# Optimization experiments

Measured on AMD Instinct MI355X. Metric: run time of the kernel, lower is better.

Reference implementation:

```python
import jax, jax.numpy as jnp
import numpy as np

N = 16384   # nodes
E = 262144  # edges (avg degree 16)
H = 256     # hidden_dim
R = 32      # num_radial


def _lin(k, fi, fo):
    return jax.random.normal(k, (fi, fo), jnp.float32) / np.float32(np.sqrt(fi))


def setup_inputs() -> dict:
    key = jax.random.key(0)
    ks = jax.random.split(key, 16)
    h = jax.random.normal(ks[0], (N, H), jnp.float32)
    pos = jax.random.normal(ks[1], (N, 3), jnp.float32)
    edge_index = jax.random.randint(ks[2], (2, E), 0, N, dtype=jnp.int32)
    return {
        'h': h, 'pos': pos,
        # radial_basis: Linear(1,R), SiLU, Linear(R,R)
        'rb_w1': _lin(ks[3], 1, R), 'rb_b1': jnp.zeros((R,), jnp.float32),
        'rb_w2': _lin(ks[4], R, R), 'rb_b2': jnp.zeros((R,), jnp.float32),
        # edge_network: Linear(2H+R,H), SiLU, Linear(H,H), LayerNorm(H)
        'en_w1': _lin(ks[5], 2 * H + R, H), 'en_b1': jnp.zeros((H,), jnp.float32),
        'en_w2': _lin(ks[6], H, H), 'en_b2': jnp.zeros((H,), jnp.float32),
        'en_g': jnp.ones((H,), jnp.float32), 'en_bt': jnp.zeros((H,), jnp.float32),
        # node_network: Linear(2H,H), SiLU, Linear(H,H), LayerNorm(H)
        'nn_w1': _lin(ks[7], 2 * H, H), 'nn_b1': jnp.zeros((H,), jnp.float32),
        'nn_w2': _lin(ks[8], H, H), 'nn_b2': jnp.zeros((H,), jnp.float32),
        'nn_g': jnp.ones((H,), jnp.float32), 'nn_bt': jnp.zeros((H,), jnp.float32),
        # coord_network: Linear(H,H//2), SiLU, Linear(H//2,1), Tanh
        'cn_w1': _lin(ks[9], H, H // 2), 'cn_b1': jnp.zeros((H // 2,), jnp.float32),
        'cn_w2': _lin(ks[10], H // 2, 1), 'cn_b2': jnp.zeros((1,), jnp.float32),
        'edge_index': edge_index,
    }


def _ln(x, g, b, eps=1e-5):
    mu = jnp.mean(x, axis=-1, keepdims=True)
    var = jnp.var(x, axis=-1, keepdims=True)
    return (x - mu) / jnp.sqrt(var + eps) * g + b


def reference(h, pos, rb_w1, rb_b1, rb_w2, rb_b2,
              en_w1, en_b1, en_w2, en_b2, en_g, en_bt,
              nn_w1, nn_b1, nn_w2, nn_b2, nn_g, nn_bt,
              cn_w1, cn_b1, cn_w2, cn_b2, edge_index):
    row, col = edge_index[0], edge_index[1]
    rel_pos = pos[col] - pos[row]                                   # [E,3]
    # torch: norm(rel_pos + 1e-8) -> scalar eps added to the vector first
    dist = jnp.linalg.norm(rel_pos + 1e-8, axis=-1, keepdims=True)  # [E,1]
    radial = jax.nn.silu(dist @ rb_w1 + rb_b1) @ rb_w2 + rb_b2      # [E,R]
    edge_feat = jnp.concatenate([h[row], h[col], radial], axis=-1)  # [E,2H+R]
    edge_msg = _ln(jax.nn.silu(edge_feat @ en_w1 + en_b1) @ en_w2 + en_b2,
                   en_g, en_bt)                                     # [E,H]
    # PyG propagate with aggr='add': sum messages at target nodes (col)
    node_msg = jax.ops.segment_sum(edge_msg, col, num_segments=h.shape[0])
    hn_in = jnp.concatenate([h, node_msg], axis=-1)                 # [N,2H]
    h_updated = _ln(jax.nn.silu(hn_in @ nn_w1 + nn_b1) @ nn_w2 + nn_b2,
                    nn_g, nn_bt)                                    # [N,H]
    coord_w = jnp.tanh(jax.nn.silu(edge_msg @ cn_w1 + cn_b1) @ cn_w2 + cn_b2)  # [E,1]
    weighted = rel_pos * coord_w                                    # [E,3]
    pos_updates = jnp.zeros_like(pos).at[row].add(-weighted).at[col].add(weighted)
    return h_updated, pos_updates
```

## Files before the change

kernel.cpp:

```cpp
#include <hip/hip_runtime.h>
#include <hip/hip_bf16.h>


#define NN 16384
#define EE 262144
#define HH 256
#define RR 32

typedef __bf16 bf16x8 __attribute__((ext_vector_type(8)));
typedef float f32x4 __attribute__((ext_vector_type(4)));

__device__ __forceinline__ float silu_f(float x) { return x / (1.0f + __expf(-x)); }

__global__ __launch_bounds__(256) void conv_h_kernel(const float* __restrict__ src,
                                                     __hip_bfloat16* __restrict__ dst,
                                                     int n4) {
  int i = blockIdx.x * 256 + threadIdx.x;
  if (i >= n4) return;
  float4 v = ((const float4*)src)[i];
  __hip_bfloat16* d = dst + (size_t)i * 4;
  d[0] = __float2bfloat16(v.x);
  d[1] = __float2bfloat16(v.y);
  d[2] = __float2bfloat16(v.z);
  d[3] = __float2bfloat16(v.w);
}

__global__ __launch_bounds__(256) void tr_kernel(const float* __restrict__ in,
                                                 __hip_bfloat16* __restrict__ out,
                                                 int K, int Nc) {
  int i = blockIdx.x * 256 + threadIdx.x;
  if (i >= K * Nc) return;
  int k = i / Nc, c = i - k * Nc;
  out[(size_t)c * K + k] = __float2bfloat16(in[i]);
}

__global__ __launch_bounds__(256) void rwt_kernel(const float* __restrict__ rb_w2,
                                                  const float* __restrict__ en_w1,
                                                  __hip_bfloat16* __restrict__ RWT) {
  int t = blockIdx.x * 256 + threadIdx.x;
  if (t >= 256 * 32) return;
  int c = t >> 5, i = t & 31;
  float s = 0.f;
#pragma unroll
  for (int j = 0; j < 32; ++j) s += rb_w2[i * 32 + j] * en_w1[(512 + j) * 256 + c];
  RWT[c * 32 + i] = __float2bfloat16(s);
}

__global__ __launch_bounds__(256) void b1p_kernel(const float* __restrict__ en_b1,
                                                  const float* __restrict__ rb_b2,
                                                  const float* __restrict__ en_w1,
                                                  float* __restrict__ b1p) {
  int c = blockIdx.x * 256 + threadIdx.x;
  if (c >= 256) return;
  float s = en_b1[c];
#pragma unroll
  for (int j = 0; j < 32; ++j) s += rb_b2[j] * en_w1[(512 + j) * 256 + c];
  b1p[c] = s;
}

__global__ __launch_bounds__(256) void count_kernel(const int* __restrict__ ei,
                                                    int* __restrict__ counts) {
  int e = blockIdx.x * 256 + threadIdx.x;
  if (e >= EE) return;
  atomicAdd(&counts[ei[EE + e]], 1);
}

__global__ __launch_bounds__(1024) void scan_kernel(const int* __restrict__ counts,
                                                    int* __restrict__ offs,
                                                    int* __restrict__ cursor) {
  __shared__ int buf[1024];
  __shared__ int carry;
  int tid = threadIdx.x;
  if (tid == 0) carry = 0;
  __syncthreads();
  for (int base = 0; base < NN; base += 1024) {
    int v = counts[base + tid];
    buf[tid] = v;
    __syncthreads();
    for (int s = 1; s < 1024; s <<= 1) {
      int x = (tid >= s) ? buf[tid - s] : 0;
      __syncthreads();
      buf[tid] += x;
      __syncthreads();
    }
    int incl = buf[tid];
    int c = carry;
    __syncthreads();
    offs[base + tid] = c + incl - v;
    cursor[base + tid] = c + incl - v;
    if (tid == 1023) carry = c + incl;
    __syncthreads();
  }
  if (tid == 0) offs[NN] = carry;
}

__global__ __launch_bounds__(256) void scatter_kernel(const int* __restrict__ ei,
                                                      int* __restrict__ cursor,
                                                      int* __restrict__ elist) {
  int e = blockIdx.x * 256 + threadIdx.x;
  if (e >= EE) return;
  int c = ei[EE + e];
  int p = atomicAdd(&cursor[c], 1);
  elist[p] = e;
}

__global__ __launch_bounds__(512) void pgemm_kernel(const __hip_bfloat16* __restrict__ A,
                                                    const __hip_bfloat16* __restrict__ BT,
                                                    __hip_bfloat16* __restrict__ out) {
  const int tid = threadIdx.x, w = tid >> 6, l = tid & 63, r = l & 15, g = l >> 4;
  const int n0 = blockIdx.x * 64;
  f32x4 acc[4][4];
#pragma unroll
  for (int a = 0; a < 4; ++a)
#pragma unroll
    for (int b = 0; b < 4; ++b) acc[a][b] = (f32x4){0.f, 0.f, 0.f, 0.f};
  for (int ks = 0; ks < 8; ++ks) {
    bf16x8 af[4], bfr[4];
#pragma unroll
    for (int fm = 0; fm < 4; ++fm)
      af[fm] = *(const bf16x8*)(A + (size_t)(n0 + fm * 16 + r) * 256 + ks * 32 + g * 8);
#pragma unroll
    for (int fn = 0; fn < 4; ++fn)
      bfr[fn] = *(const bf16x8*)(BT + (size_t)(w * 64 + fn * 16 + r) * 256 + ks * 32 + g * 8);
#pragma unroll
    for (int fm = 0; fm < 4; ++fm)
#pragma unroll
      for (int fn = 0; fn < 4; ++fn)
        acc[fm][fn] =
            __builtin_amdgcn_mfma_f32_16x16x32_bf16(af[fm], bfr[fn], acc[fm][fn], 0, 0, 0);
  }
#pragma unroll
  for (int fm = 0; fm < 4; ++fm)
#pragma unroll
    for (int fn = 0; fn < 4; ++fn) {
      int col = w * 64 + fn * 16 + r;
#pragma unroll
      for (int q = 0; q < 4; ++q) {
        int row = n0 + fm * 16 + g * 4 + q;
        out[(size_t)row * 512 + col] = __float2bfloat16(acc[fm][fn][q]);
      }
    }
}

__global__ __launch_bounds__(512, 4) void edge_kernel(
    const __hip_bfloat16* __restrict__ Pb, const int* __restrict__ ei,
    const float* __restrict__ pos, const float* __restrict__ rb_w1,
    const float* __restrict__ rb_b1, const __hip_bfloat16* __restrict__ RWT,
    const float* __restrict__ b1p, const __hip_bfloat16* __restrict__ W2T,
    const float* __restrict__ en_b2, const float* __restrict__ en_g,
    const float* __restrict__ en_bt, const __hip_bfloat16* __restrict__ CW1T,
    const float* __restrict__ cn_b1, const float* __restrict__ cn_w2,
    const float* __restrict__ cn_b2, __hip_bfloat16* __restrict__ emsg,
    float* __restrict__ pos_out) {
  __shared__ __align__(16) __hip_bfloat16 A2[64 * 264];
  __shared__ float distb[64];
  __shared__ float relb[64][3];
  __shared__ int srow[64], scol[64];
  __shared__ float wc1[32], bc1[32];
  __shared__ float red[8][64], redsq[8][64], red2[8][64];
  __shared__ float mv[64][2];
  __shared__ float gb[HH], btb[HH], cb1b[128], cw2b[128];

  const int tid = threadIdx.x, w = tid >> 6, l = tid & 63, r = l & 15, g = l >> 4;
  const int e0 = blockIdx.x * 64;

  if (tid < 256) {
    gb[tid] = en_g[tid];
    btb[tid] = en_bt[tid];
  }
  if (tid < 128) {
    cb1b[tid] = cn_b1[tid];
    cw2b[tid] = cn_w2[tid];
  }
  if (tid < 32) {
    wc1[tid] = rb_w1[tid];
    bc1[tid] = rb_b1[tid];
  }
  if (tid < 64) {
    int e = e0 + tid;
    int rr = ei[e], cc = ei[EE + e];
    srow[tid] = rr;
    scol[tid] = cc;
    float dx = pos[cc * 3 + 0] - pos[rr * 3 + 0];
    float dy = pos[cc * 3 + 1] - pos[rr * 3 + 1];
    float dz = pos[cc * 3 + 2] - pos[rr * 3 + 2];
    relb[tid][0] = dx;
    relb[tid][1] = dy;
    relb[tid][2] = dz;
    float ex = dx + 1e-8f, ey = dy + 1e-8f, ez = dz + 1e-8f;
    distb[tid] = sqrtf(ex * ex + ey * ey + ez * ez);
  }
  __syncthreads();

#pragma unroll
  for (int it = 0; it < 4; ++it) {
    int ch = it * 512 + tid;
    int i = ch >> 5, c = ch & 31;
    bf16x8 p1 = *(const bf16x8*)(Pb + (size_t)srow[i] * 512 + c * 8);
    bf16x8 p2 = *(const bf16x8*)(Pb + (size_t)scol[i] * 512 + 256 + c * 8);
    bf16x8 o;
#pragma unroll
    for (int j = 0; j < 8; ++j) o[j] = (__bf16)((float)p1[j] + (float)p2[j]);
    *(bf16x8*)(A2 + i * 264 + c * 8) = o;
  }

  f32x4 acc[4][2];
  {
    bf16x8 sf[4], bfr[2];
#pragma unroll
    for (int fm = 0; fm < 4; ++fm) {
      float d = distb[fm * 16 + r];
      bf16x8 v;
#pragma unroll
      for (int j = 0; j < 8; ++j) {
        float x = d * wc1[g * 8 + j] + bc1[g * 8 + j];
        v[j] = (__bf16)silu_f(x);
      }
      sf[fm] = v;
    }
#pragma unroll
    for (int fn = 0; fn < 2; ++fn)
      bfr[fn] = *(const bf16x8*)(RWT + (size_t)(w * 32 + fn * 16 + r) * 32 + g * 8);
#pragma unroll
    for (int fm = 0; fm < 4; ++fm)
#pragma unroll
      for (int fn = 0; fn < 2; ++fn)
        acc[fm][fn] = __builtin_amdgcn_mfma_f32_16x16x32_bf16(
            sf[fm], bfr[fn], (f32x4){0.f, 0.f, 0.f, 0.f}, 0, 0, 0);
  }
  __syncthreads();

#pragma unroll
  for (int fn = 0; fn < 2; ++fn) {
    int col = w * 32 + fn * 16 + r;
    float bp = b1p[col];
#pragma unroll
    for (int fm = 0; fm < 4; ++fm)
#pragma unroll
      for (int q = 0; q < 4; ++q) {
        int row = fm * 16 + g * 4 + q;
        float ps = __bfloat162float(A2[row * 264 + col]);
        A2[row * 264 + col] = __float2bfloat16(silu_f(acc[fm][fn][q] + ps + bp));
      }
  }
  __syncthreads();

#pragma unroll
  for (int a = 0; a < 4; ++a)
#pragma unroll
    for (int b = 0; b < 2; ++b) acc[a][b] = (f32x4){0.f, 0.f, 0.f, 0.f};
  for (int ks = 0; ks < 8; ++ks) {
    bf16x8 af[4], bfr[2];
#pragma unroll
    for (int fm = 0; fm < 4; ++fm)
      af[fm] = *(const bf16x8*)(A2 + (fm * 16 + r) * 264 + ks * 32 + g * 8);
#pragma unroll
    for (int fn = 0; fn < 2; ++fn)
      bfr[fn] = *(const bf16x8*)(W2T + (size_t)(w * 32 + fn * 16 + r) * 256 + ks * 32 + g * 8);
#pragma unroll
    for (int fm = 0; fm < 4; ++fm)
#pragma unroll
      for (int fn = 0; fn < 2; ++fn)
        acc[fm][fn] =
            __builtin_amdgcn_mfma_f32_16x16x32_bf16(af[fm], bfr[fn], acc[fm][fn], 0, 0, 0);
  }
#pragma unroll
  for (int fn = 0; fn < 2; ++fn) {
    float b2 = en_b2[w * 32 + fn * 16 + r];
#pragma unroll
    for (int fm = 0; fm < 4; ++fm)
#pragma unroll
      for (int q = 0; q < 4; ++q) acc[fm][fn][q] += b2;
  }

#pragma unroll
  for (int fm = 0; fm < 4; ++fm)
#pragma unroll
    for (int q = 0; q < 4; ++q) {
      float s = acc[fm][0][q] + acc[fm][1][q];
      float sq = acc[fm][0][q] * acc[fm][0][q] + acc[fm][1][q] * acc[fm][1][q];
#pragma unroll
      for (int m = 1; m < 16; m <<= 1) {
        s += __shfl_xor(s, m, 64);
        sq += __shfl_xor(sq, m, 64);
      }
      if (r == 0) {
        red[w][fm * 16 + g * 4 + q] = s;
        redsq[w][fm * 16 + g * 4 + q] = sq;
      }
    }
  __syncthreads();
  if (tid < 64) {
    float s = 0.f, sq = 0.f;
#pragma unroll
    for (int k = 0; k < 8; ++k) {
      s += red[k][tid];
      sq += redsq[k][tid];
    }
    float mean = s * (1.0f / HH);
    float var = sq * (1.0f / HH) - mean * mean;
    mv[tid][0] = mean;
    mv[tid][1] = rsqrtf(var + 1e-5f);
  }
  __syncthreads();
#pragma unroll
  for (int fn = 0; fn < 2; ++fn) {
    int col = w * 32 + fn * 16 + r;
    float gg = gb[col], bb = btb[col];
#pragma unroll
    for (int fm = 0; fm < 4; ++fm)
#pragma unroll
      for (int q = 0; q < 4; ++q) {
        int row = fm * 16 + g * 4 + q;
        A2[row * 264 + col] =
            __float2bfloat16((acc[fm][fn][q] - mv[row][0]) * mv[row][1] * gg + bb);
      }
  }
  __syncthreads();

#pragma unroll
  for (int it = 0; it < 4; ++it) {
    int ch = it * 512 + tid;
    int i = ch >> 5, c = ch & 31;
    *(float4*)(emsg + (size_t)(e0 + i) * HH + c * 8) = *(const float4*)(A2 + i * 264 + c * 8);
  }

  f32x4 c2[4];
#pragma unroll
  for (int a = 0; a < 4; ++a) c2[a] = (f32x4){0.f, 0.f, 0.f, 0.f};
  for (int ks = 0; ks < 8; ++ks) {
    bf16x8 af[4];
#pragma unroll
    for (int fm = 0; fm < 4; ++fm)
      af[fm] = *(const bf16x8*)(A2 + (fm * 16 + r) * 264 + ks * 32 + g * 8);
    bf16x8 bfr = *(const bf16x8*)(CW1T + (size_t)(w * 16 + r) * 256 + ks * 32 + g * 8);
#pragma unroll
    for (int fm = 0; fm < 4; ++fm)
      c2[fm] = __builtin_amdgcn_mfma_f32_16x16x32_bf16(af[fm], bfr, c2[fm], 0, 0, 0);
  }
  {
    int ccol = w * 16 + r;
    float cb = cb1b[ccol], cw = cw2b[ccol];
#pragma unroll
    for (int fm = 0; fm < 4; ++fm)
#pragma unroll
      for (int q = 0; q < 4; ++q) {
        float v = silu_f(c2[fm][q] + cb) * cw;
#pragma unroll
        for (int m = 1; m < 16; m <<= 1) v += __shfl_xor(v, m, 64);
        if (r == 0) red2[w][fm * 16 + g * 4 + q] = v;
      }
  }
  __syncthreads();
  if (tid < 64) {
    float s = cn_b2[0];
#pragma unroll
    for (int k = 0; k < 8; ++k) s += red2[k][tid];
    float wgt = tanhf(s);
    float ax = relb[tid][0], ay = relb[tid][1], az = relb[tid][2];
    int rr = srow[tid], cc = scol[tid];
    atomicAdd(&pos_out[rr * 3 + 0], -wgt * ax);
    atomicAdd(&pos_out[rr * 3 + 1], -wgt * ay);
    atomicAdd(&pos_out[rr * 3 + 2], -wgt * az);
    atomicAdd(&pos_out[cc * 3 + 0], wgt * ax);
    atomicAdd(&pos_out[cc * 3 + 1], wgt * ay);
    atomicAdd(&pos_out[cc * 3 + 2], wgt * az);
  }
}

__global__ __launch_bounds__(256) void nodemsg_kernel(const int* __restrict__ offs,
                                                      const int* __restrict__ elist,
                                                      const __hip_bfloat16* __restrict__ emsg,
                                                      __hip_bfloat16* __restrict__ nmsgb) {
  int wid = threadIdx.x >> 6, l = threadIdx.x & 63;
  int n = blockIdx.x * 4 + wid;
  float a0 = 0.f, a1 = 0.f, a2 = 0.f, a3 = 0.f;
  int b = offs[n], e2 = offs[n + 1];
  for (int idx = b; idx < e2; ++idx) {
    int e = elist[idx];
    const __hip_bfloat16* row = emsg + (size_t)e * HH;
    a0 += __bfloat162float(row[l]);
    a1 += __bfloat162float(row[l + 64]);
    a2 += __bfloat162float(row[l + 128]);
    a3 += __bfloat162float(row[l + 192]);
  }
  __hip_bfloat16* out = nmsgb + (size_t)n * HH;
  out[l] = __float2bfloat16(a0);
  out[l + 64] = __float2bfloat16(a1);
  out[l + 128] = __float2bfloat16(a2);
  out[l + 192] = __float2bfloat16(a3);
}

__global__ __launch_bounds__(512, 4) void node_kernel(
    const __hip_bfloat16* __restrict__ hb, const __hip_bfloat16* __restrict__ nmsgb,
    const __hip_bfloat16* __restrict__ NW1T, const float* __restrict__ nn_b1,
    const __hip_bfloat16* __restrict__ NW2T, const float* __restrict__ nn_b2,
    const float* __restrict__ nn_g, const float* __restrict__ nn_bt,
    float* __restrict__ out_h) {
  __shared__ __align__(16) __hip_bfloat16 A2[32 * 264];
  __shared__ float red[8][32], redsq[8][32];
  __shared__ float mv[32][2];
  __shared__ float gb[HH], btb[HH];
  const int tid = threadIdx.x, w = tid >> 6, l = tid & 63, r = l & 15, g = l >> 4;
  const int n0 = blockIdx.x * 32;
  if (tid < 256) {
    gb[tid] = nn_g[tid];
    btb[tid] = nn_bt[tid];
  }

  f32x4 acc[2][2];
#pragma unroll
  for (int a = 0; a < 2; ++a)
#pragma unroll
    for (int b = 0; b < 2; ++b) acc[a][b] = (f32x4){0.f, 0.f, 0.f, 0.f};
  for (int ks = 0; ks < 8; ++ks) {
    bf16x8 af[2], bfr[2];
#pragma unroll
    for (int fm = 0; fm < 2; ++fm)
      af[fm] = *(const bf16x8*)(hb + (size_t)(n0 + fm * 16 + r) * 256 + ks * 32 + g * 8);
#pragma unroll
    for (int fn = 0; fn < 2; ++fn)
      bfr[fn] = *(const bf16x8*)(NW1T + (size_t)(w * 32 + fn * 16 + r) * 512 + ks * 32 + g * 8);
#pragma unroll
    for (int fm = 0; fm < 2; ++fm)
#pragma unroll
      for (int fn = 0; fn < 2; ++fn)
        acc[fm][fn] =
            __builtin_amdgcn_mfma_f32_16x16x32_bf16(af[fm], bfr[fn], acc[fm][fn], 0, 0, 0);
  }
  for (int ks = 0; ks < 8; ++ks) {
    bf16x8 af[2], bfr[2];
#pragma unroll
    for (int fm = 0; fm < 2; ++fm)
      af[fm] = *(const bf16x8*)(nmsgb + (size_t)(n0 + fm * 16 + r) * 256 + ks * 32 + g * 8);
#pragma unroll
    for (int fn = 0; fn < 2; ++fn)
      bfr[fn] = *(const bf16x8*)(NW1T + (size_t)(w * 32 + fn * 16 + r) * 512 + 256 + ks * 32 + g * 8);
#pragma unroll
    for (int fm = 0; fm < 2; ++fm)
#pragma unroll
      for (int fn = 0; fn < 2; ++fn)
        acc[fm][fn] =
            __builtin_amdgcn_mfma_f32_16x16x32_bf16(af[fm], bfr[fn], acc[fm][fn], 0, 0, 0);
  }
  __syncthreads();
#pragma unroll
  for (int fn = 0; fn < 2; ++fn) {
    int col = w * 32 + fn * 16 + r;
    float b1 = nn_b1[col];
#pragma unroll
    for (int fm = 0; fm < 2; ++fm)
#pragma unroll
      for (int q = 0; q < 4; ++q) {
        int row = fm * 16 + g * 4 + q;
        A2[row * 264 + col] = __float2bfloat16(silu_f(acc[fm][fn][q] + b1));
      }
  }
  __syncthreads();

#pragma unroll
  for (int a = 0; a < 2; ++a)
#pragma unroll
    for (int b = 0; b < 2; ++b) acc[a][b] = (f32x4){0.f, 0.f, 0.f, 0.f};
  for (int ks = 0; ks < 8; ++ks) {
    bf16x8 af[2], bfr[2];
#pragma unroll
    for (int fm = 0; fm < 2; ++fm)
      af[fm] = *(const bf16x8*)(A2 + (fm * 16 + r) * 264 + ks * 32 + g * 8);
#pragma unroll
    for (int fn = 0; fn < 2; ++fn)
      bfr[fn] = *(const bf16x8*)(NW2T + (size_t)(w * 32 + fn * 16 + r) * 256 + ks * 32 + g * 8);
#pragma unroll
    for (int fm = 0; fm < 2; ++fm)
#pragma unroll
      for (int fn = 0; fn < 2; ++fn)
        acc[fm][fn] =
            __builtin_amdgcn_mfma_f32_16x16x32_bf16(af[fm], bfr[fn], acc[fm][fn], 0, 0, 0);
  }
#pragma unroll
  for (int fn = 0; fn < 2; ++fn) {
    float b2 = nn_b2[w * 32 + fn * 16 + r];
#pragma unroll
    for (int fm = 0; fm < 2; ++fm)
#pragma unroll
      for (int q = 0; q < 4; ++q) acc[fm][fn][q] += b2;
  }
#pragma unroll
  for (int fm = 0; fm < 2; ++fm)
#pragma unroll
    for (int q = 0; q < 4; ++q) {
      float s = acc[fm][0][q] + acc[fm][1][q];
      float sq = acc[fm][0][q] * acc[fm][0][q] + acc[fm][1][q] * acc[fm][1][q];
#pragma unroll
      for (int m = 1; m < 16; m <<= 1) {
        s += __shfl_xor(s, m, 64);
        sq += __shfl_xor(sq, m, 64);
      }
      if (r == 0) {
        red[w][fm * 16 + g * 4 + q] = s;
        redsq[w][fm * 16 + g * 4 + q] = sq;
      }
    }
  __syncthreads();
  if (tid < 32) {
    float s = 0.f, sq = 0.f;
#pragma unroll
    for (int k = 0; k < 8; ++k) {
      s += red[k][tid];
      sq += redsq[k][tid];
    }
    float mean = s * (1.0f / HH);
    float var = sq * (1.0f / HH) - mean * mean;
    mv[tid][0] = mean;
    mv[tid][1] = rsqrtf(var + 1e-5f);
  }
  __syncthreads();
#pragma unroll
  for (int fn = 0; fn < 2; ++fn) {
    int col = w * 32 + fn * 16 + r;
    float gg = gb[col], bb = btb[col];
#pragma unroll
    for (int fm = 0; fm < 2; ++fm)
#pragma unroll
      for (int q = 0; q < 4; ++q) {
        int row = fm * 16 + g * 4 + q;
        out_h[(size_t)(n0 + row) * HH + col] =
            (acc[fm][fn][q] - mv[row][0]) * mv[row][1] * gg + bb;
      }
  }
}

extern "C" void kernel_launch(void* const* d_in, const int* in_sizes, int n_in,
                              void* d_out, int out_size, void* d_ws, size_t ws_size,
                              hipStream_t stream) {
  const float* h = (const float*)d_in[0];
  const float* pos = (const float*)d_in[1];
  const float* rb_w1 = (const float*)d_in[2];
  const float* rb_b1 = (const float*)d_in[3];
  const float* rb_w2 = (const float*)d_in[4];
  const float* rb_b2 = (const float*)d_in[5];
  const float* en_w1 = (const float*)d_in[6];
  const float* en_b1 = (const float*)d_in[7];
  const float* en_w2 = (const float*)d_in[8];
  const float* en_b2 = (const float*)d_in[9];
  const float* en_g = (const float*)d_in[10];
  const float* en_bt = (const float*)d_in[11];
  const float* nn_w1 = (const float*)d_in[12];
  const float* nn_b1 = (const float*)d_in[13];
  const float* nn_w2 = (const float*)d_in[14];
  const float* nn_b2 = (const float*)d_in[15];
  const float* nn_g = (const float*)d_in[16];
  const float* nn_bt = (const float*)d_in[17];
  const float* cn_w1 = (const float*)d_in[18];
  const float* cn_b1 = (const float*)d_in[19];
  const float* cn_w2 = (const float*)d_in[20];
  const float* cn_b2 = (const float*)d_in[21];
  const int* ei = (const int*)d_in[22];

  float* out_h = (float*)d_out;
  float* out_pos = out_h + (size_t)NN * HH;

  char* p = (char*)d_ws;
  auto alloc = [&p](size_t bytes) {
    char* q = p;
    p += (bytes + 255) & ~(size_t)255;
    return q;
  };
  __hip_bfloat16* hb = (__hip_bfloat16*)alloc((size_t)NN * HH * 2);
  __hip_bfloat16* Pb = (__hip_bfloat16*)alloc((size_t)NN * 512 * 2);
  __hip_bfloat16* W1abT = (__hip_bfloat16*)alloc((size_t)512 * 256 * 2);
  __hip_bfloat16* W2T = (__hip_bfloat16*)alloc((size_t)256 * 256 * 2);
  __hip_bfloat16* NW1T = (__hip_bfloat16*)alloc((size_t)256 * 512 * 2);
  __hip_bfloat16* NW2T = (__hip_bfloat16*)alloc((size_t)256 * 256 * 2);
  __hip_bfloat16* CW1T = (__hip_bfloat16*)alloc((size_t)128 * 256 * 2);
  __hip_bfloat16* RWT = (__hip_bfloat16*)alloc((size_t)256 * 32 * 2);
  float* b1p = (float*)alloc((size_t)256 * 4);
  __hip_bfloat16* emsg = (__hip_bfloat16*)alloc((size_t)EE * HH * 2);
  __hip_bfloat16* nmsgb = (__hip_bfloat16*)alloc((size_t)NN * HH * 2);
  int* counts = (int*)alloc((size_t)NN * 4);
  int* offs = (int*)alloc((size_t)(NN + 1) * 4);
  int* cursor = (int*)alloc((size_t)NN * 4);
  int* elist = (int*)alloc((size_t)EE * 4);

  hipMemsetAsync(out_pos, 0, (size_t)NN * 3 * sizeof(float), stream);
  hipMemsetAsync(counts, 0, (size_t)NN * sizeof(int), stream);

  conv_h_kernel<<<(NN * HH / 4 + 255) / 256, 256, 0, stream>>>(h, hb, NN * HH / 4);
  tr_kernel<<<(256 * 256) / 256, 256, 0, stream>>>(en_w2, W2T, 256, 256);
  tr_kernel<<<(512 * 256) / 256, 256, 0, stream>>>(nn_w1, NW1T, 512, 256);
  tr_kernel<<<(256 * 256) / 256, 256, 0, stream>>>(nn_w2, NW2T, 256, 256);
  tr_kernel<<<(256 * 128) / 256, 256, 0, stream>>>(cn_w1, CW1T, 256, 128);
  tr_kernel<<<(256 * 256) / 256, 256, 0, stream>>>(en_w1, W1abT, 256, 256);
  tr_kernel<<<(256 * 256) / 256, 256, 0, stream>>>(en_w1 + 256 * 256, W1abT + 256 * 256, 256,
                                                   256);
  rwt_kernel<<<(256 * 32) / 256, 256, 0, stream>>>(rb_w2, en_w1, RWT);
  b1p_kernel<<<1, 256, 0, stream>>>(en_b1, rb_b2, en_w1, b1p);
  count_kernel<<<EE / 256, 256, 0, stream>>>(ei, counts);
  scan_kernel<<<1, 1024, 0, stream>>>(counts, offs, cursor);
  scatter_kernel<<<EE / 256, 256, 0, stream>>>(ei, cursor, elist);
  pgemm_kernel<<<NN / 64, 512, 0, stream>>>(hb, W1abT, Pb);
  edge_kernel<<<EE / 64, 512, 0, stream>>>(Pb, ei, pos, rb_w1, rb_b1, RWT, b1p, W2T, en_b2,
                                           en_g, en_bt, CW1T, cn_b1, cn_w2, cn_b2, emsg,
                                           out_pos);
  nodemsg_kernel<<<NN / 4, 256, 0, stream>>>(offs, elist, emsg, nmsgb);
  node_kernel<<<NN / 32, 512, 0, stream>>>(hb, nmsgb, NW1T, nn_b1, NW2T, nn_b2, nn_g, nn_bt,
                                           out_h);
}
```

Baseline: 526.1 us.

## Fuse radial MFMA into edge gather, parallelize scan, vectorize node message sum

```diff
diff --git a/kernel.cpp b/kernel.cpp
--- a/kernel.cpp
+++ b/kernel.cpp
@@ -11,6 +11,15 @@
 typedef float f32x4 __attribute__((ext_vector_type(4)));
 
 __device__ __forceinline__ float silu_f(float x) { return x / (1.0f + __expf(-x)); }
+
+__device__ __forceinline__ unsigned short bf_bits(float x) {
+  union { __hip_bfloat16 b; unsigned short u; } v;
+  v.b = __float2bfloat16(x);
+  return v.u;
+}
+__device__ __forceinline__ float ubf(unsigned short u) {
+  return __uint_as_float(((unsigned)u) << 16);
+}
 
 __global__ __launch_bounds__(256) void conv_h_kernel(const float* __restrict__ src,
                                                      __hip_bfloat16* __restrict__ dst,
@@ -65,33 +74,52 @@
   atomicAdd(&counts[ei[EE + e]], 1);
 }
 
-__global__ __launch_bounds__(1024) void scan_kernel(const int* __restrict__ counts,
+__global__ __launch_bounds__(256) void scanA_kernel(const int* __restrict__ counts,
+                                                    int* __restrict__ bsum) {
+  __shared__ int ws[4];
+  int t = threadIdx.x;
+  int v = counts[blockIdx.x * 256 + t];
+#pragma unroll
+  for (int m = 1; m < 64; m <<= 1) v += __shfl_xor(v, m, 64);
+  if ((t & 63) == 0) ws[t >> 6] = v;
+  __syncthreads();
+  if (t == 0) bsum[blockIdx.x] = ws[0] + ws[1] + ws[2] + ws[3];
+}
+
+__global__ __launch_bounds__(64) void scanB_kernel(const int* __restrict__ bsum,
+                                                   int* __restrict__ bbase,
+                                                   int* __restrict__ offs) {
+  int t = threadIdx.x;
+  int v = bsum[t], x = v;
+#pragma unroll
+  for (int d = 1; d < 64; d <<= 1) {
+    int y = __shfl_up(x, d, 64);
+    if (t >= d) x += y;
+  }
+  bbase[t] = x - v;
+  if (t == 63) offs[NN] = x;
+}
+
+__global__ __launch_bounds__(256) void scanC_kernel(const int* __restrict__ counts,
+                                                    const int* __restrict__ bbase,
                                                     int* __restrict__ offs,
                                                     int* __restrict__ cursor) {
-  __shared__ int buf[1024];
-  __shared__ int carry;
-  int tid = threadIdx.x;
-  if (tid == 0) carry = 0;
-  __syncthreads();
-  for (int base = 0; base < NN; base += 1024) {
-    int v = counts[base + tid];
-    buf[tid] = v;
-    __syncthreads();
-    for (int s = 1; s < 1024; s <<= 1) {
-      int x = (tid >= s) ? buf[tid - s] : 0;
-      __syncthreads();
-      buf[tid] += x;
-      __syncthreads();
-    }
-    int incl = buf[tid];
-    int c = carry;
-    __syncthreads();
-    offs[base + tid] = c + incl - v;
-    cursor[base + tid] = c + incl - v;
-    if (tid == 1023) carry = c + incl;
-    __syncthreads();
-  }
-  if (tid == 0) offs[NN] = carry;
+  __shared__ int wtot[4];
+  int t = threadIdx.x, wv = t >> 6, ln = t & 63;
+  int base = blockIdx.x * 256;
+  int v = counts[base + t], x = v;
+#pragma unroll
+  for (int d = 1; d < 64; d <<= 1) {
+    int y = __shfl_up(x, d, 64);
+    if (ln >= d) x += y;
+  }
+  if (ln == 63) wtot[wv] = x;
+  __syncthreads();
+  int add = bbase[blockIdx.x];
+  for (int k = 0; k < wv; ++k) add += wtot[k];
+  int excl = add + x - v;
+  offs[base + t] = excl;
+  cursor[base + t] = excl;
 }
 
 __global__ __launch_bounds__(256) void scatter_kernel(const int* __restrict__ ei,
@@ -153,16 +181,29 @@
     const float* __restrict__ cn_b2, __hip_bfloat16* __restrict__ emsg,
     float* __restrict__ pos_out) {
   __shared__ __align__(16) __hip_bfloat16 A2[64 * 264];
-  __shared__ float distb[64];
   __shared__ float relb[64][3];
   __shared__ int srow[64], scol[64];
-  __shared__ float wc1[32], bc1[32];
-  __shared__ float red[8][64], redsq[8][64], red2[8][64];
+  __shared__ float red[8][64], redsq[8][64];
   __shared__ float mv[64][2];
   __shared__ float gb[HH], btb[HH], cb1b[128], cw2b[128];
 
   const int tid = threadIdx.x, w = tid >> 6, l = tid & 63, r = l & 15, g = l >> 4;
   const int e0 = blockIdx.x * 64;
+  const int chalf = w >> 2;
+
+  const int eloc = (w & 3) * 16 + r;
+  const int eg = e0 + eloc;
+  const int nr = ei[eg], nc = ei[EE + eg];
+  float dx = pos[nc * 3 + 0] - pos[nr * 3 + 0] + 1e-8f;
+  float dy = pos[nc * 3 + 1] - pos[nr * 3 + 1] + 1e-8f;
+  float dz = pos[nc * 3 + 2] - pos[nr * 3 + 2] + 1e-8f;
+  float d = sqrtf(dx * dx + dy * dy + dz * dz);
+  bf16x8 sfrag;
+#pragma unroll
+  for (int j = 0; j < 8; ++j) {
+    float x = d * rb_w1[g * 8 + j] + rb_b1[g * 8 + j];
+    sfrag[j] = (__bf16)silu_f(x);
+  }
 
   if (tid < 256) {
     gb[tid] = en_g[tid];
@@ -172,79 +213,38 @@
     cb1b[tid] = cn_b1[tid];
     cw2b[tid] = cn_w2[tid];
   }
-  if (tid < 32) {
-    wc1[tid] = rb_w1[tid];
-    bc1[tid] = rb_b1[tid];
-  }
   if (tid < 64) {
     int e = e0 + tid;
-    int rr = ei[e], cc = ei[EE + e];
-    srow[tid] = rr;
-    scol[tid] = cc;
-    float dx = pos[cc * 3 + 0] - pos[rr * 3 + 0];
-    float dy = pos[cc * 3 + 1] - pos[rr * 3 + 1];
-    float dz = pos[cc * 3 + 2] - pos[rr * 3 + 2];
-    relb[tid][0] = dx;
-    relb[tid][1] = dy;
-    relb[tid][2] = dz;
-    float ex = dx + 1e-8f, ey = dy + 1e-8f, ez = dz + 1e-8f;
-    distb[tid] = sqrtf(ex * ex + ey * ey + ez * ez);
-  }
-  __syncthreads();
-
-#pragma unroll
-  for (int it = 0; it < 4; ++it) {
-    int ch = it * 512 + tid;
-    int i = ch >> 5, c = ch & 31;
-    bf16x8 p1 = *(const bf16x8*)(Pb + (size_t)srow[i] * 512 + c * 8);
-    bf16x8 p2 = *(const bf16x8*)(Pb + (size_t)scol[i] * 512 + 256 + c * 8);
-    bf16x8 o;
-#pragma unroll
-    for (int j = 0; j < 8; ++j) o[j] = (__bf16)((float)p1[j] + (float)p2[j]);
-    *(bf16x8*)(A2 + i * 264 + c * 8) = o;
-  }
+    int r2 = ei[e], c2 = ei[EE + e];
+    srow[tid] = r2;
+    scol[tid] = c2;
+    relb[tid][0] = pos[c2 * 3 + 0] - pos[r2 * 3 + 0];
+    relb[tid][1] = pos[c2 * 3 + 1] - pos[r2 * 3 + 1];
+    relb[tid][2] = pos[c2 * 3 + 2] - pos[r2 * 3 + 2];
+  }
+
+  const unsigned short* Pu = (const unsigned short*)Pb;
+  unsigned short* A2u = (unsigned short*)A2;
+#pragma unroll
+  for (int t = 0; t < 8; ++t) {
+    int cblk = chalf * 8 + t;
+    int cbase = cblk * 16 + g * 4;
+    bf16x8 afr = *(const bf16x8*)(RWT + (size_t)(cblk * 16 + r) * 32 + g * 8);
+    f32x4 rad = __builtin_amdgcn_mfma_f32_16x16x32_bf16(afr, sfrag,
+                                                        (f32x4){0.f, 0.f, 0.f, 0.f}, 0, 0, 0);
+    ushort4 p1 = *(const ushort4*)(Pu + (size_t)nr * 512 + cbase);
+    ushort4 p2 = *(const ushort4*)(Pu + (size_t)nc * 512 + 256 + cbase);
+    float4 b1v = *(const float4*)(b1p + cbase);
+    ushort4 o;
+    o.x = bf_bits(silu_f(rad[0] + ubf(p1.x) + ubf(p2.x) + b1v.x));
+    o.y = bf_bits(silu_f(rad[1] + ubf(p1.y) + ubf(p2.y) + b1v.y));
+    o.z = bf_bits(silu_f(rad[2] + ubf(p1.z) + ubf(p2.z) + b1v.z));
+    o.w = bf_bits(silu_f(rad[3] + ubf(p1.w) + ubf(p2.w) + b1v.w));
+    *(ushort4*)(A2u + (size_t)eloc * 264 + cbase) = o;
+  }
+  __syncthreads();
 
   f32x4 acc[4][2];
-  {
-    bf16x8 sf[4], bfr[2];
-#pragma unroll
-    for (int fm = 0; fm < 4; ++fm) {
-      float d = distb[fm * 16 + r];
-      bf16x8 v;
-#pragma unroll
-      for (int j = 0; j < 8; ++j) {
-        float x = d * wc1[g * 8 + j] + bc1[g * 8 + j];
-        v[j] = (__bf16)silu_f(x);
-      }
-      sf[fm] = v;
-    }
-#pragma unroll
-    for (int fn = 0; fn < 2; ++fn)
-      bfr[fn] = *(const bf16x8*)(RWT + (size_t)(w * 32 + fn * 16 + r) * 32 + g * 8);
-#pragma unroll
-    for (int fm = 0; fm < 4; ++fm)
-#pragma unroll
-      for (int fn = 0; fn < 2; ++fn)
-        acc[fm][fn] = __builtin_amdgcn_mfma_f32_16x16x32_bf16(
-            sf[fm], bfr[fn], (f32x4){0.f, 0.f, 0.f, 0.f}, 0, 0, 0);
-  }
-  __syncthreads();
-
-#pragma unroll
-  for (int fn = 0; fn < 2; ++fn) {
-    int col = w * 32 + fn * 16 + r;
-    float bp = b1p[col];
-#pragma unroll
-    for (int fm = 0; fm < 4; ++fm)
-#pragma unroll
-      for (int q = 0; q < 4; ++q) {
-        int row = fm * 16 + g * 4 + q;
-        float ps = __bfloat162float(A2[row * 264 + col]);
-        A2[row * 264 + col] = __float2bfloat16(silu_f(acc[fm][fn][q] + ps + bp));
-      }
-  }
-  __syncthreads();
-
 #pragma unroll
   for (int a = 0; a < 4; ++a)
 #pragma unroll
@@ -325,9 +325,9 @@
     *(float4*)(emsg + (size_t)(e0 + i) * HH + c * 8) = *(const float4*)(A2 + i * 264 + c * 8);
   }
 
-  f32x4 c2[4];
-#pragma unroll
-  for (int a = 0; a < 4; ++a) c2[a] = (f32x4){0.f, 0.f, 0.f, 0.f};
+  f32x4 c2a[4];
+#pragma unroll
+  for (int a = 0; a < 4; ++a) c2a[a] = (f32x4){0.f, 0.f, 0.f, 0.f};
   for (int ks = 0; ks < 8; ++ks) {
     bf16x8 af[4];
 #pragma unroll
@@ -336,7 +336,7 @@
     bf16x8 bfr = *(const bf16x8*)(CW1T + (size_t)(w * 16 + r) * 256 + ks * 32 + g * 8);
 #pragma unroll
     for (int fm = 0; fm < 4; ++fm)
-      c2[fm] = __builtin_amdgcn_mfma_f32_16x16x32_bf16(af[fm], bfr, c2[fm], 0, 0, 0);
+      c2a[fm] = __builtin_amdgcn_mfma_f32_16x16x32_bf16(af[fm], bfr, c2a[fm], 0, 0, 0);
   }
   {
     int ccol = w * 16 + r;
@@ -345,17 +345,17 @@
     for (int fm = 0; fm < 4; ++fm)
 #pragma unroll
       for (int q = 0; q < 4; ++q) {
-        float v = silu_f(c2[fm][q] + cb) * cw;
+        float v = silu_f(c2a[fm][q] + cb) * cw;
 #pragma unroll
         for (int m = 1; m < 16; m <<= 1) v += __shfl_xor(v, m, 64);
-        if (r == 0) red2[w][fm * 16 + g * 4 + q] = v;
+        if (r == 0) red[w][fm * 16 + g * 4 + q] = v;
       }
   }
   __syncthreads();
   if (tid < 64) {
     float s = cn_b2[0];
 #pragma unroll
-    for (int k = 0; k < 8; ++k) s += red2[k][tid];
+    for (int k = 0; k < 8; ++k) s += red[k][tid];
     float wgt = tanhf(s);
     float ax = relb[tid][0], ay = relb[tid][1], az = relb[tid][2];
     int rr = srow[tid], cc = scol[tid];
@@ -376,19 +376,31 @@
   int n = blockIdx.x * 4 + wid;
   float a0 = 0.f, a1 = 0.f, a2 = 0.f, a3 = 0.f;
   int b = offs[n], e2 = offs[n + 1];
-  for (int idx = b; idx < e2; ++idx) {
-    int e = elist[idx];
-    const __hip_bfloat16* row = emsg + (size_t)e * HH;
-    a0 += __bfloat162float(row[l]);
-    a1 += __bfloat162float(row[l + 64]);
-    a2 += __bfloat162float(row[l + 128]);
-    a3 += __bfloat162float(row[l + 192]);
-  }
-  __hip_bfloat16* out = nmsgb + (size_t)n * HH;
-  out[l] = __float2bfloat16(a0);
-  out[l + 64] = __float2bfloat16(a1);
-  out[l + 128] = __float2bfloat16(a2);
-  out[l + 192] = __float2bfloat16(a3);
+  const unsigned short* E = (const unsigned short*)emsg;
+  int idx = b;
+  for (; idx + 1 < e2; idx += 2) {
+    int ea = elist[idx], eb = elist[idx + 1];
+    ushort4 va = *(const ushort4*)(E + (size_t)ea * HH + l * 4);
+    ushort4 vb = *(const ushort4*)(E + (size_t)eb * HH + l * 4);
+    a0 += ubf(va.x) + ubf(vb.x);
+    a1 += ubf(va.y) + ubf(vb.y);
+    a2 += ubf(va.z) + ubf(vb.z);
+    a3 += ubf(va.w) + ubf(vb.w);
+  }
+  if (idx < e2) {
+    int ea = elist[idx];
+    ushort4 va = *(const ushort4*)(E + (size_t)ea * HH + l * 4);
+    a0 += ubf(va.x);
+    a1 += ubf(va.y);
+    a2 += ubf(va.z);
+    a3 += ubf(va.w);
+  }
+  ushort4 o;
+  o.x = bf_bits(a0);
+  o.y = bf_bits(a1);
+  o.z = bf_bits(a2);
+  o.w = bf_bits(a3);
+  *(ushort4*)((unsigned short*)nmsgb + (size_t)n * HH + l * 4) = o;
 }
 
 __global__ __launch_bounds__(512, 4) void node_kernel(
@@ -435,7 +447,8 @@
       af[fm] = *(const bf16x8*)(nmsgb + (size_t)(n0 + fm * 16 + r) * 256 + ks * 32 + g * 8);
 #pragma unroll
     for (int fn = 0; fn < 2; ++fn)
-      bfr[fn] = *(const bf16x8*)(NW1T + (size_t)(w * 32 + fn * 16 + r) * 512 + 256 + ks * 32 + g * 8);
+      bfr[fn] =
+          *(const bf16x8*)(NW1T + (size_t)(w * 32 + fn * 16 + r) * 512 + 256 + ks * 32 + g * 8);
 #pragma unroll
     for (int fm = 0; fm < 2; ++fm)
 #pragma unroll
@@ -581,6 +594,8 @@
   int* offs = (int*)alloc((size_t)(NN + 1) * 4);
   int* cursor = (int*)alloc((size_t)NN * 4);
   int* elist = (int*)alloc((size_t)EE * 4);
+  int* bsum = (int*)alloc((size_t)64 * 4);
+  int* bbase = (int*)alloc((size_t)64 * 4);
 
   hipMemsetAsync(out_pos, 0, (size_t)NN * 3 * sizeof(float), stream);
   hipMemsetAsync(counts, 0, (size_t)NN * sizeof(int), stream);
@@ -596,7 +611,9 @@
   rwt_kernel<<<(256 * 32) / 256, 256, 0, stream>>>(rb_w2, en_w1, RWT);
   b1p_kernel<<<1, 256, 0, stream>>>(en_b1, rb_b2, en_w1, b1p);
   count_kernel<<<EE / 256, 256, 0, stream>>>(ei, counts);
-  scan_kernel<<<1, 1024, 0, stream>>>(counts, offs, cursor);
+  scanA_kernel<<<NN / 256, 256, 0, stream>>>(counts, bsum);
+  scanB_kernel<<<1, 64, 0, stream>>>(bsum, bbase, offs);
+  scanC_kernel<<<NN / 256, 256, 0, stream>>>(counts, bbase, offs, cursor);
   scatter_kernel<<<EE / 256, 256, 0, stream>>>(ei, cursor, elist);
   pgemm_kernel<<<NN / 64, 512, 0, stream>>>(hb, W1abT, Pb);
   edge_kernel<<<EE / 64, 512, 0, stream>>>(Pb, ei, pos, rb_w1, rb_b1, RWT, b1p, W2T, en_b2,
```

Measured after the change: 521.4 us. About the same (-0.9%).
